# Optimization experiments

Hardware: AMD Instinct MI355X
Metric: run time of the kernel (lower is better)

The kernel has to match this reference:

```python
import jax, jax.numpy as jnp
import numpy as np

N_NODES = 50000
N_EDGES = 800000
IN_FEAT = 256
OUT_FEAT = 256
NUM_RELS = 8
NUM_BASES = 4


def setup_inputs() -> dict:
    key = jax.random.key(0)
    ks = jax.random.split(key, 8)
    feat = jax.random.normal(ks[0], (N_NODES, IN_FEAT), dtype=jnp.float32)
    norm = jax.random.uniform(ks[1], (N_EDGES, 1), dtype=jnp.float32)
    src = jax.random.randint(ks[2], (N_EDGES,), 0, N_NODES)
    dst = jax.random.randint(ks[3], (N_EDGES,), 0, N_NODES)
    etypes = jax.random.randint(ks[4], (N_EDGES,), 0, NUM_RELS)
    # learned parameters (xavier-ish scale)
    weight = jax.random.normal(ks[5], (NUM_BASES, IN_FEAT, OUT_FEAT), dtype=jnp.float32) * (2.0 / np.sqrt(IN_FEAT + OUT_FEAT))
    w_comp = jax.random.normal(ks[6], (NUM_RELS, NUM_BASES), dtype=jnp.float32) * (2.0 / np.sqrt(NUM_RELS + NUM_BASES))
    loop_weight = jax.random.normal(ks[7], (IN_FEAT, OUT_FEAT), dtype=jnp.float32) * (2.0 / np.sqrt(IN_FEAT + OUT_FEAT))
    h_bias = jnp.zeros((OUT_FEAT,), dtype=jnp.float32)
    return {"feat": feat, "weight": weight, "w_comp": w_comp,
            "loop_weight": loop_weight, "h_bias": h_bias,
            "norm": norm, "src": src, "dst": dst, "etypes": etypes}


def reference(feat, weight, w_comp, loop_weight, h_bias, norm, src, dst, etypes):
    # basis decomposition: W_r = sum_b a_{rb} V_b  -> [R, in, out]
    W = jnp.einsum('rb,bio->rio', w_comp, weight)
    # relation-grouped GEMM: transform every node by every relation. [N, R, out]
    Hr = jnp.einsum('ni,rio->nro', feat, W)
    # per-edge message: gather (src node, edge relation) then apply edge norm. [E, out]
    msg = Hr[src, etypes] * norm
    # scatter-reduce (sum) messages to destination nodes. [N, out]
    agg = jax.ops.segment_sum(msg, dst, num_segments=N_NODES)
    # self-loop + bias + activation (dropout rate 0.0 -> identity)
    out = agg + feat @ loop_weight + h_bias
    return jax.nn.relu(out)
```

## Files before the change

### kernel.cpp

```cpp
#include <hip/hip_runtime.h>
#include <stdint.h>

typedef unsigned short u16;
typedef __bf16 bf16x8 __attribute__((ext_vector_type(8)));
typedef float f32x4 __attribute__((ext_vector_type(4)));

#define N_NODES 50000
#define N_PAD   50048
#define NUM_E   800000
#define FDIM    256
#define NREL    8
#define NSEG    (N_NODES * NREL)
#define NBLK    391
#define MTILES  196

#define PREP_FEAT_BLOCKS 12512
#define PREP_WT_BLOCKS   2304
#define PREP_ZERO_BLOCKS 1563

__device__ __forceinline__ u16 f2bf(float f) {
  uint32_t u = __float_as_uint(f);
  u += 0x7FFFu + ((u >> 16) & 1u);
  return (u16)(u >> 16);
}
__device__ __forceinline__ float bf2f(u16 h) {
  return __uint_as_float(((uint32_t)h) << 16);
}

__device__ __forceinline__ void gload_lds16(const void* g, void* l) {
  __builtin_amdgcn_global_load_lds(
      (__attribute__((address_space(1))) uint32_t*)(void*)(uintptr_t)g,
      (__attribute__((address_space(3))) uint32_t*)(uintptr_t)l,
      16, 0, 0);
}

__global__ __launch_bounds__(256) void prep_k(const float* __restrict__ feat,
                                              const float* __restrict__ weight,
                                              const float* __restrict__ w_comp,
                                              const float* __restrict__ loop_w,
                                              u16* __restrict__ fb,
                                              u16* __restrict__ W_all,
                                              int* __restrict__ cnt) {
  const int b = blockIdx.x;
  const int tid = threadIdx.x;
  if (b < PREP_FEAT_BLOCKS) {
    int idx = b * 256 + tid;
    int row = idx >> 6;
    int q = (idx & 63) * 4;
    float4 v = make_float4(0.f, 0.f, 0.f, 0.f);
    if (row < N_NODES) v = *reinterpret_cast<const float4*>(feat + (size_t)row * FDIM + q);
    ushort4 h;
    h.x = f2bf(v.x); h.y = f2bf(v.y); h.z = f2bf(v.z); h.w = f2bf(v.w);
    *reinterpret_cast<ushort4*>(fb + (size_t)row * FDIM + q) = h;
  } else if (b < PREP_FEAT_BLOCKS + PREP_WT_BLOCKS) {
    int idx = (b - PREP_FEAT_BLOCKS) * 256 + tid;
    if (idx < NREL * 65536) {
      int r = idx >> 16, rem = idx & 65535;
      int o = rem >> 8, i = rem & 255;
      float s = 0.f;
#pragma unroll
      for (int bb = 0; bb < 4; ++bb)
        s += w_comp[r * 4 + bb] * weight[bb * 65536 + i * 256 + o];
      W_all[idx] = f2bf(s);
    } else {
      int j = idx - NREL * 65536;
      int o = j >> 8, i = j & 255;
      W_all[idx] = f2bf(loop_w[i * 256 + o]);
    }
  } else {
    int i = (b - PREP_FEAT_BLOCKS - PREP_WT_BLOCKS) * 256 + tid;
    if (i < NSEG) cnt[i] = 0;
  }
}

__global__ __launch_bounds__(256) void hist_k(const int* __restrict__ dst,
                                              const int* __restrict__ et,
                                              int* __restrict__ cnt) {
  int e = blockIdx.x * 256 + threadIdx.x;
  if (e < NUM_E) atomicAdd(&cnt[dst[e] * NREL + et[e]], 1);
}

__global__ __launch_bounds__(1024) void scan1(const int* __restrict__ cnt,
                                              int* __restrict__ rowstart,
                                              int* __restrict__ blocksum) {
  __shared__ int wtot[16], woff[16];
  const int tid = threadIdx.x, lane = tid & 63, w = tid >> 6;
  const int i = blockIdx.x * 1024 + tid;
  const int v = (i < NSEG) ? cnt[i] : 0;
  int inc = v;
#pragma unroll
  for (int off = 1; off < 64; off <<= 1) {
    int t = __shfl_up(inc, off);
    if (lane >= off) inc += t;
  }
  if (lane == 63) wtot[w] = inc;
  __syncthreads();
  if (w == 0) {
    int tv = (lane < 16) ? wtot[lane] : 0;
    int tinc = tv;
#pragma unroll
    for (int off = 1; off < 16; off <<= 1) {
      int t = __shfl_up(tinc, off);
      if (lane >= off) tinc += t;
    }
    if (lane < 16) woff[lane] = tinc - tv;
    if (lane == 15) blocksum[blockIdx.x] = tinc;
  }
  __syncthreads();
  if (i < NSEG) rowstart[i] = inc - v + woff[w];
}

__global__ __launch_bounds__(512) void scan2(int* __restrict__ blocksum) {
  __shared__ int s[512];
  const int tid = threadIdx.x;
  const int v = (tid < NBLK) ? blocksum[tid] : 0;
  s[tid] = v;
#pragma unroll
  for (int off = 1; off < 512; off <<= 1) {
    __syncthreads();
    int t = (tid >= off) ? s[tid - off] : 0;
    __syncthreads();
    s[tid] += t;
  }
  if (tid < NBLK) blocksum[tid] = s[tid] - v;
}

__global__ __launch_bounds__(1024) void scan3(int* __restrict__ rowstart,
                                              const int* __restrict__ blockoff,
                                              int* __restrict__ cursor) {
  const int i = blockIdx.x * 1024 + threadIdx.x;
  if (i < NSEG) {
    const int v = rowstart[i] + blockoff[i >> 10];
    rowstart[i] = v;
    cursor[i] = v;
  }
  if (i == NSEG) rowstart[NSEG] = NUM_E;
}

__global__ __launch_bounds__(256) void bucket_k(const int* __restrict__ src,
                                                const int* __restrict__ dst,
                                                const int* __restrict__ et,
                                                const float* __restrict__ norm,
                                                int* __restrict__ cursor,
                                                int* __restrict__ keys,
                                                float* __restrict__ norms) {
  int e = blockIdx.x * 256 + threadIdx.x;
  if (e >= NUM_E) return;
  const int pos = atomicAdd(&cursor[dst[e] * NREL + et[e]], 1);
  keys[pos]  = src[e];
  norms[pos] = norm[e];
}

__global__ __launch_bounds__(256) void agg_T(const u16* __restrict__ feat_bf,
                                             const int* __restrict__ rowstart,
                                             const int* __restrict__ keys,
                                             const float* __restrict__ norms,
                                             u16* __restrict__ T) {
  const int n = blockIdx.x * 4 + (threadIdx.x >> 6);
  if (n >= N_NODES) return;
  const int lane = threadIdx.x & 63;
  int rsv = 0;
  if (lane < 9) rsv = rowstart[n * NREL + lane];
  f32x4 acc[8] = {};
#pragma unroll
  for (int r = 0; r < 8; ++r) {
    const int b = __shfl(rsv, r), e = __shfl(rsv, r + 1);
    for (int base = b; base < e; base += 64) {
      const int m = min(64, e - base);
      int kv = 0; float nv = 0.f;
      if (lane < m) { kv = keys[base + lane]; nv = norms[base + lane]; }
      for (int j = 0; j < m; ++j) {
        const int s = __shfl(kv, j);
        const float nm = __shfl(nv, j);
        const ushort4 h = *reinterpret_cast<const ushort4*>(
            feat_bf + (size_t)s * FDIM + lane * 4);
        acc[r][0] += bf2f(h.x) * nm;
        acc[r][1] += bf2f(h.y) * nm;
        acc[r][2] += bf2f(h.z) * nm;
        acc[r][3] += bf2f(h.w) * nm;
      }
    }
  }
#pragma unroll
  for (int r = 0; r < 8; ++r) {
    ushort4 hh;
    hh.x = f2bf(acc[r][0]);
    hh.y = f2bf(acc[r][1]);
    hh.z = f2bf(acc[r][2]);
    hh.w = f2bf(acc[r][3]);
    *reinterpret_cast<ushort4*>(T + (size_t)n * (NREL * FDIM) + r * FDIM + lane * 4) = hh;
  }
}

__global__ __launch_bounds__(512, 2) void fused_gemm(const u16* __restrict__ T,
                                                     const u16* __restrict__ feat_bf,
                                                     const u16* __restrict__ W_all,
                                                     const float* __restrict__ bias,
                                                     float* __restrict__ out) {
  __shared__ __align__(16) u16 As[2][256 * 64];
  __shared__ __align__(16) u16 Bs[2][256 * 64];
  const int tid = threadIdx.x;
  const int lane = tid & 63;
  const int w = tid >> 6;
  const int wm = w >> 2, wn = w & 3;
  const int mtile = blockIdx.x;

  const int srow = tid >> 3;
  const int scolx = ((tid & 7) << 3) ^ ((srow & 7) << 3);

  f32x4 acc[8][4] = {};

  auto stage = [&](int ks, int buf) {
    const int r = ks >> 2, kk4 = ks & 3;
    const int kcol = kk4 * 64 + scolx;
#pragma unroll
    for (int q = 0; q < 4; ++q) {
      const int arow = q * 64 + srow;
      int gr = mtile * 256 + arow;
      if (gr >= N_PAD) gr = N_PAD - 1;
      const u16* asrc = (r < 8)
          ? T + (size_t)gr * 2048 + r * 256 + kcol
          : feat_bf + (size_t)gr * 256 + kcol;
      gload_lds16(asrc, &As[buf][q * 4096 + tid * 8]);
      const u16* bsrc = W_all + (size_t)r * 65536 + (size_t)arow * 256 + kcol;
      gload_lds16(bsrc, &Bs[buf][q * 4096 + tid * 8]);
    }
  };

  stage(0, 0);
  __syncthreads();
  for (int t = 0; t < 36; ++t) {
    const int cur = t & 1;
    if (t + 1 < 36) stage(t + 1, cur ^ 1);
#pragma unroll
    for (int kk = 0; kk < 2; ++kk) {
      const int colx = (kk * 32 + ((lane >> 4) << 3)) ^ ((lane & 7) << 3);
      bf16x8 a[8], b[4];
#pragma unroll
      for (int mf = 0; mf < 8; ++mf)
        a[mf] = *reinterpret_cast<const bf16x8*>(
            &As[cur][(wm * 128 + mf * 16 + (lane & 15)) * 64 + colx]);
#pragma unroll
      for (int nf = 0; nf < 4; ++nf)
        b[nf] = *reinterpret_cast<const bf16x8*>(
            &Bs[cur][(wn * 64 + nf * 16 + (lane & 15)) * 64 + colx]);
      __builtin_amdgcn_s_setprio(1);
#pragma unroll
      for (int mf = 0; mf < 8; ++mf)
#pragma unroll
        for (int nf = 0; nf < 4; ++nf)
          acc[mf][nf] = __builtin_amdgcn_mfma_f32_16x16x32_bf16(b[nf], a[mf], acc[mf][nf], 0, 0, 0);
      __builtin_amdgcn_s_setprio(0);
    }
    __syncthreads();
  }

#pragma unroll
  for (int mf = 0; mf < 8; ++mf) {
    const int m = mtile * 256 + wm * 128 + mf * 16 + (lane & 15);
    if (m >= N_NODES) continue;
#pragma unroll
    for (int nf = 0; nf < 4; ++nf) {
      const int o0 = wn * 64 + nf * 16 + ((lane >> 4) << 2);
      const float4 bv = *reinterpret_cast<const float4*>(bias + o0);
      float4 v;
      v.x = fmaxf(acc[mf][nf][0] + bv.x, 0.f);
      v.y = fmaxf(acc[mf][nf][1] + bv.y, 0.f);
      v.z = fmaxf(acc[mf][nf][2] + bv.z, 0.f);
      v.w = fmaxf(acc[mf][nf][3] + bv.w, 0.f);
      *reinterpret_cast<float4*>(out + (size_t)m * 256 + o0) = v;
    }
  }
}

extern "C" void kernel_launch(void* const* d_in, const int* in_sizes, int n_in,
                              void* d_out, int out_size, void* d_ws, size_t ws_size,
                              hipStream_t stream) {
  (void)in_sizes; (void)n_in; (void)out_size; (void)ws_size;
  const float* feat   = (const float*)d_in[0];
  const float* weight = (const float*)d_in[1];
  const float* w_comp = (const float*)d_in[2];
  const float* loop_w = (const float*)d_in[3];
  const float* h_bias = (const float*)d_in[4];
  const float* norm   = (const float*)d_in[5];
  const int*   src    = (const int*)d_in[6];
  const int*   dst    = (const int*)d_in[7];
  const int*   et     = (const int*)d_in[8];
  float* out = (float*)d_out;

  char* ws = (char*)d_ws;
  u16*   feat_bf  = (u16*)(ws);
  u16*   W_all    = (u16*)(ws + 25624576);
  u16*   T        = (u16*)(ws + 26804224);
  int*   counts   = (int*)(ws + 231804928);
  int*   rowstart = (int*)(ws + 233404928);
  int*   cursor   = (int*)(ws + 235005184);
  int*   keys     = (int*)(ws + 236605184);
  float* norms    = (float*)(ws + 239805184);
  int*   blocksum = (int*)(ws + 243005184);

  prep_k<<<PREP_FEAT_BLOCKS + PREP_WT_BLOCKS + PREP_ZERO_BLOCKS, 256, 0, stream>>>(
      feat, weight, w_comp, loop_w, feat_bf, W_all, counts);

  hist_k<<<(NUM_E + 255) / 256, 256, 0, stream>>>(dst, et, counts);
  scan1<<<NBLK, 1024, 0, stream>>>(counts, rowstart, blocksum);
  scan2<<<1, 512, 0, stream>>>(blocksum);
  scan3<<<NBLK + 1, 1024, 0, stream>>>(rowstart, blocksum, cursor);
  bucket_k<<<(NUM_E + 255) / 256, 256, 0, stream>>>(src, dst, et, norm, cursor, keys, norms);

  agg_T<<<(N_NODES + 3) / 4, 256, 0, stream>>>(feat_bf, rowstart, keys, norms, T);

  fused_gemm<<<MTILES, 512, 0, stream>>>(T, feat_bf, W_all, h_bias, out);
}
```

Measured before the change: 278.9 us.

## Aggregate per basis instead of per relation to shrink GEMM K dimension

Folds the basis coefficients into the edge aggregation, so each node accumulates 4 basis-weighted sums instead of 8 relation sums. The GEMM then runs over 5 K-blocks (4 bases plus self-loop) instead of 9, and the intermediate buffer is halved. CSR bucketing now uses per-node segments with the edge type packed into the key, which shrinks the scan. The aggregation also software-prefetches the next gathered row. In exchange it does more FMAs per edge and reads coefficients from LDS.

```diff
diff --git a/kernel.cpp b/kernel.cpp
--- a/kernel.cpp
+++ b/kernel.cpp
@@ -10,13 +10,16 @@
 #define NUM_E   800000
 #define FDIM    256
 #define NREL    8
-#define NSEG    (N_NODES * NREL)
-#define NBLK    391
+#define NBASE   4
+#define KBLK    5
+#define NKSTEP  20
+#define NSEG    N_NODES
+#define NBLK    49
 #define MTILES  196
 
 #define PREP_FEAT_BLOCKS 12512
-#define PREP_WT_BLOCKS   2304
-#define PREP_ZERO_BLOCKS 1563
+#define PREP_WT_BLOCKS   1280
+#define PREP_ZERO_BLOCKS 196
 
 __device__ __forceinline__ u16 f2bf(float f) {
   uint32_t u = __float_as_uint(f);
@@ -36,10 +39,9 @@
 
 __global__ __launch_bounds__(256) void prep_k(const float* __restrict__ feat,
                                               const float* __restrict__ weight,
-                                              const float* __restrict__ w_comp,
                                               const float* __restrict__ loop_w,
                                               u16* __restrict__ fb,
-                                              u16* __restrict__ W_all,
+                                              u16* __restrict__ Wb_all,
                                               int* __restrict__ cnt) {
   const int b = blockIdx.x;
   const int tid = threadIdx.x;
@@ -54,19 +56,11 @@
     *reinterpret_cast<ushort4*>(fb + (size_t)row * FDIM + q) = h;
   } else if (b < PREP_FEAT_BLOCKS + PREP_WT_BLOCKS) {
     int idx = (b - PREP_FEAT_BLOCKS) * 256 + tid;
-    if (idx < NREL * 65536) {
-      int r = idx >> 16, rem = idx & 65535;
-      int o = rem >> 8, i = rem & 255;
-      float s = 0.f;
-#pragma unroll
-      for (int bb = 0; bb < 4; ++bb)
-        s += w_comp[r * 4 + bb] * weight[bb * 65536 + i * 256 + o];
-      W_all[idx] = f2bf(s);
-    } else {
-      int j = idx - NREL * 65536;
-      int o = j >> 8, i = j & 255;
-      W_all[idx] = f2bf(loop_w[i * 256 + o]);
-    }
+    int r = idx >> 16, rem = idx & 65535;
+    int o = rem >> 8, i = rem & 255;
+    float s = (r < NBASE) ? weight[(size_t)r * 65536 + i * 256 + o]
+                          : loop_w[i * 256 + o];
+    Wb_all[idx] = f2bf(s);
   } else {
     int i = (b - PREP_FEAT_BLOCKS - PREP_WT_BLOCKS) * 256 + tid;
     if (i < NSEG) cnt[i] = 0;
@@ -74,10 +68,9 @@
 }
 
 __global__ __launch_bounds__(256) void hist_k(const int* __restrict__ dst,
-                                              const int* __restrict__ et,
                                               int* __restrict__ cnt) {
   int e = blockIdx.x * 256 + threadIdx.x;
-  if (e < NUM_E) atomicAdd(&cnt[dst[e] * NREL + et[e]], 1);
+  if (e < NUM_E) atomicAdd(&cnt[dst[e]], 1);
 }
 
 __global__ __launch_bounds__(1024) void scan1(const int* __restrict__ cnt,
@@ -146,55 +139,68 @@
                                                 float* __restrict__ norms) {
   int e = blockIdx.x * 256 + threadIdx.x;
   if (e >= NUM_E) return;
-  const int pos = atomicAdd(&cursor[dst[e] * NREL + et[e]], 1);
-  keys[pos]  = src[e];
+  const int pos = atomicAdd(&cursor[dst[e]], 1);
+  keys[pos]  = src[e] * NREL + et[e];
   norms[pos] = norm[e];
 }
 
-__global__ __launch_bounds__(256) void agg_T(const u16* __restrict__ feat_bf,
+__global__ __launch_bounds__(256) void agg_G(const u16* __restrict__ feat_bf,
                                              const int* __restrict__ rowstart,
                                              const int* __restrict__ keys,
                                              const float* __restrict__ norms,
-                                             u16* __restrict__ T) {
+                                             const float* __restrict__ w_comp,
+                                             u16* __restrict__ G) {
+  __shared__ float wcs[NREL * NBASE];
+  if (threadIdx.x < NREL * NBASE) wcs[threadIdx.x] = w_comp[threadIdx.x];
+  __syncthreads();
   const int n = blockIdx.x * 4 + (threadIdx.x >> 6);
-  if (n >= N_NODES) return;
   const int lane = threadIdx.x & 63;
-  int rsv = 0;
-  if (lane < 9) rsv = rowstart[n * NREL + lane];
-  f32x4 acc[8] = {};
-#pragma unroll
-  for (int r = 0; r < 8; ++r) {
-    const int b = __shfl(rsv, r), e = __shfl(rsv, r + 1);
-    for (int base = b; base < e; base += 64) {
-      const int m = min(64, e - base);
-      int kv = 0; float nv = 0.f;
-      if (lane < m) { kv = keys[base + lane]; nv = norms[base + lane]; }
-      for (int j = 0; j < m; ++j) {
-        const int s = __shfl(kv, j);
-        const float nm = __shfl(nv, j);
-        const ushort4 h = *reinterpret_cast<const ushort4*>(
-            feat_bf + (size_t)s * FDIM + lane * 4);
-        acc[r][0] += bf2f(h.x) * nm;
-        acc[r][1] += bf2f(h.y) * nm;
-        acc[r][2] += bf2f(h.z) * nm;
-        acc[r][3] += bf2f(h.w) * nm;
+  const int beg = rowstart[n], end = rowstart[n + 1];
+
+  f32x4 acc[NBASE] = {};
+  for (int base = beg; base < end; base += 64) {
+    const int m = min(64, end - base);
+    int kv = 0; float nv = 0.f;
+    if (lane < m) { kv = keys[base + lane]; nv = norms[base + lane]; }
+    int key = __shfl(kv, 0);
+    float nm = __shfl(nv, 0);
+    ushort4 h = *reinterpret_cast<const ushort4*>(
+        feat_bf + (size_t)(key >> 3) * FDIM + lane * 4);
+    for (int j = 0; j < m; ++j) {
+      ushort4 h2; int key2 = 0; float nm2 = 0.f;
+      if (j + 1 < m) {
+        key2 = __shfl(kv, j + 1);
+        nm2 = __shfl(nv, j + 1);
+        h2 = *reinterpret_cast<const ushort4*>(
+            feat_bf + (size_t)(key2 >> 3) * FDIM + lane * 4);
       }
-    }
-  }
-#pragma unroll
-  for (int r = 0; r < 8; ++r) {
+      const int et = key & 7;
+      const float f0 = bf2f(h.x), f1 = bf2f(h.y), f2 = bf2f(h.z), f3 = bf2f(h.w);
+#pragma unroll
+      for (int bb = 0; bb < NBASE; ++bb) {
+        const float c = nm * wcs[et * NBASE + bb];
+        acc[bb][0] += f0 * c;
+        acc[bb][1] += f1 * c;
+        acc[bb][2] += f2 * c;
+        acc[bb][3] += f3 * c;
+      }
+      h = h2; key = key2; nm = nm2;
+    }
+  }
+#pragma unroll
+  for (int bb = 0; bb < NBASE; ++bb) {
     ushort4 hh;
-    hh.x = f2bf(acc[r][0]);
-    hh.y = f2bf(acc[r][1]);
-    hh.z = f2bf(acc[r][2]);
-    hh.w = f2bf(acc[r][3]);
-    *reinterpret_cast<ushort4*>(T + (size_t)n * (NREL * FDIM) + r * FDIM + lane * 4) = hh;
-  }
-}
-
-__global__ __launch_bounds__(512, 2) void fused_gemm(const u16* __restrict__ T,
+    hh.x = f2bf(acc[bb][0]);
+    hh.y = f2bf(acc[bb][1]);
+    hh.z = f2bf(acc[bb][2]);
+    hh.w = f2bf(acc[bb][3]);
+    *reinterpret_cast<ushort4*>(G + (size_t)n * (NBASE * FDIM) + bb * FDIM + lane * 4) = hh;
+  }
+}
+
+__global__ __launch_bounds__(512, 2) void fused_gemm(const u16* __restrict__ G,
                                                      const u16* __restrict__ feat_bf,
-                                                     const u16* __restrict__ W_all,
+                                                     const u16* __restrict__ Wb_all,
                                                      const float* __restrict__ bias,
                                                      float* __restrict__ out) {
   __shared__ __align__(16) u16 As[2][256 * 64];
@@ -218,20 +224,20 @@
       const int arow = q * 64 + srow;
       int gr = mtile * 256 + arow;
       if (gr >= N_PAD) gr = N_PAD - 1;
-      const u16* asrc = (r < 8)
-          ? T + (size_t)gr * 2048 + r * 256 + kcol
+      const u16* asrc = (r < NBASE)
+          ? G + (size_t)gr * 1024 + r * 256 + kcol
           : feat_bf + (size_t)gr * 256 + kcol;
       gload_lds16(asrc, &As[buf][q * 4096 + tid * 8]);
-      const u16* bsrc = W_all + (size_t)r * 65536 + (size_t)arow * 256 + kcol;
+      const u16* bsrc = Wb_all + (size_t)r * 65536 + (size_t)arow * 256 + kcol;
       gload_lds16(bsrc, &Bs[buf][q * 4096 + tid * 8]);
     }
   };
 
   stage(0, 0);
   __syncthreads();
-  for (int t = 0; t < 36; ++t) {
+  for (int t = 0; t < NKSTEP; ++t) {
     const int cur = t & 1;
-    if (t + 1 < 36) stage(t + 1, cur ^ 1);
+    if (t + 1 < NKSTEP) stage(t + 1, cur ^ 1);
 #pragma unroll
     for (int kk = 0; kk < 2; ++kk) {
       const int colx = (kk * 32 + ((lane >> 4) << 3)) ^ ((lane & 7) << 3);
@@ -290,25 +296,25 @@
 
   char* ws = (char*)d_ws;
   u16*   feat_bf  = (u16*)(ws);
-  u16*   W_all    = (u16*)(ws + 25624576);
-  u16*   T        = (u16*)(ws + 26804224);
-  int*   counts   = (int*)(ws + 231804928);
-  int*   rowstart = (int*)(ws + 233404928);
-  int*   cursor   = (int*)(ws + 235005184);
-  int*   keys     = (int*)(ws + 236605184);
-  float* norms    = (float*)(ws + 239805184);
-  int*   blocksum = (int*)(ws + 243005184);
+  u16*   Wb_all   = (u16*)(ws + 25624576);
+  u16*   G        = (u16*)(ws + 26279936);
+  int*   counts   = (int*)(ws + 128778240);
+  int*   rowstart = (int*)(ws + 128978432);
+  int*   cursor   = (int*)(ws + 129178880);
+  int*   keys     = (int*)(ws + 129379072);
+  float* norms    = (float*)(ws + 132579072);
+  int*   blocksum = (int*)(ws + 135779072);
 
   prep_k<<<PREP_FEAT_BLOCKS + PREP_WT_BLOCKS + PREP_ZERO_BLOCKS, 256, 0, stream>>>(
-      feat, weight, w_comp, loop_w, feat_bf, W_all, counts);
-
-  hist_k<<<(NUM_E + 255) / 256, 256, 0, stream>>>(dst, et, counts);
+      feat, weight, loop_w, feat_bf, Wb_all, counts);
+
+  hist_k<<<(NUM_E + 255) / 256, 256, 0, stream>>>(dst, counts);
   scan1<<<NBLK, 1024, 0, stream>>>(counts, rowstart, blocksum);
   scan2<<<1, 512, 0, stream>>>(blocksum);
   scan3<<<NBLK + 1, 1024, 0, stream>>>(rowstart, blocksum, cursor);
   bucket_k<<<(NUM_E + 255) / 256, 256, 0, stream>>>(src, dst, et, norm, cursor, keys, norms);
 
-  agg_T<<<(N_NODES + 3) / 4, 256, 0, stream>>>(feat_bf, rowstart, keys, norms, T);
-
-  fused_gemm<<<MTILES, 512, 0, stream>>>(T, feat_bf, W_all, h_bias, out);
-}
+  agg_G<<<N_NODES / 4, 256, 0, stream>>>(feat_bf, rowstart, keys, norms, w_comp, G);
+
+  fused_gemm<<<MTILES, 512, 0, stream>>>(G, feat_bf, Wb_all, h_bias, out);
+}
```

Result: faster. 229.1 us (-17.9%).
